# Performance work log

Hardware: AMD Instinct MI355X
Metric: run time of the kernel (lower is better)

The kernel has to match this reference:

```python
import jax, jax.numpy as jnp
import numpy as np

T, B, D, H = 512, 128, 512, 512


def setup_inputs() -> dict:
    key = jax.random.key(0)
    ks = jax.random.split(key, 14)
    s = 0.05
    return {
        "inputs": jax.random.normal(ks[0], (T, B, D), dtype=jnp.float32),
        # gate linears: Linear(D+H, out) -> weight [out, D+H], bias [out]
        "Wf": jax.random.normal(ks[1], (2, D + H), dtype=jnp.float32) * s,
        "bf": jax.random.normal(ks[2], (2,), dtype=jnp.float32) * s,
        "Wi": jax.random.normal(ks[3], (H, D + H), dtype=jnp.float32) * s,
        "bi": jax.random.normal(ks[4], (H,), dtype=jnp.float32) * s,
        "Wu": jax.random.normal(ks[5], (H, D + H), dtype=jnp.float32) * s,
        "bu": jax.random.normal(ks[6], (H,), dtype=jnp.float32) * s,
        "Wo": jax.random.normal(ks[7], (H, D + H), dtype=jnp.float32) * s,
        "bo": jax.random.normal(ks[8], (H,), dtype=jnp.float32) * s,
        # SamplerModule: Linear(2,4) -> Tanh -> Linear(4,2) -> softmax
        "Ws1": jax.random.normal(ks[9], (4, 2), dtype=jnp.float32) * 0.5,
        "bs1": jax.random.normal(ks[10], (4,), dtype=jnp.float32) * 0.5,
        "Ws2": jax.random.normal(ks[11], (2, 4), dtype=jnp.float32) * 0.5,
        "bs2": jax.random.normal(ks[12], (2,), dtype=jnp.float32) * 0.5,
    }


def reference(inputs, Wf, bf, Wi, bi, Wu, bu, Wo, bo, Ws1, bs1, Ws2, bs2):
    Bsz = inputs.shape[1]
    h0 = jnp.zeros((Bsz, H), dtype=inputs.dtype)
    c0 = jnp.zeros((Bsz, H), dtype=inputs.dtype)

    def step(carry, x):
        hx, cx = carry
        combined = jnp.concatenate([x, hx], axis=1)  # [B, D+H]
        f_logits = combined @ Wf.T + bf              # [B, 2]
        hdn = jnp.tanh(f_logits @ Ws1.T + bs1)       # [B, 4]
        f_probs = jax.nn.softmax(hdn @ Ws2.T + bs2, axis=-1)  # [B, 2]
        f = f_probs[:, 0:1]                          # [B, 1] forget gate
        i = jax.nn.sigmoid(combined @ Wi.T + bi)
        g = jnp.tanh(combined @ Wu.T + bu)
        o = jax.nn.sigmoid(combined @ Wo.T + bo)
        cx = f * cx + i * g
        hx = o * jnp.tanh(cx)
        return (hx, cx), hx

    (hx, cx), stacked = jax.lax.scan(step, (h0, c0), inputs)
    return stacked, (hx, cx)
```

## Files before the change

### kernel.cpp

```cpp
#include <hip/hip_runtime.h>
#include <cstdint>

#define TT 512
#define BB 128
#define DD 512
#define HH 512
#define KTOT 1024
#define LDK 1032

typedef short bf16x8 __attribute__((ext_vector_type(8)));
typedef float f32x4 __attribute__((ext_vector_type(4)));

__device__ inline unsigned short f2bfs(float f) {
    unsigned int u = __builtin_bit_cast(unsigned int, f);
    u = (u + 0x7FFFu + ((u >> 16) & 1u)) >> 16;
    return (unsigned short)u;
}

__device__ inline float sigf(float x) { return 1.f / (1.f + __expf(-x)); }
__device__ inline float tanhfast(float x) { return 2.f * sigf(2.f * x) - 1.f; }

__device__ inline bf16x8 load8w(const float* p) {
    const float4* p4 = (const float4*)p;
    float4 a = p4[0], b = p4[1];
    bf16x8 r;
    r[0] = (short)f2bfs(a.x); r[1] = (short)f2bfs(a.y);
    r[2] = (short)f2bfs(a.z); r[3] = (short)f2bfs(a.w);
    r[4] = (short)f2bfs(b.x); r[5] = (short)f2bfs(b.y);
    r[6] = (short)f2bfs(b.z); r[7] = (short)f2bfs(b.w);
    return r;
}

__global__ __launch_bounds__(256, 1) void qlstm_kernel(
    const float* __restrict__ X,
    const float* __restrict__ Wf, const float* __restrict__ bfb,
    const float* __restrict__ Wi, const float* __restrict__ bi,
    const float* __restrict__ Wu, const float* __restrict__ bu,
    const float* __restrict__ Wo, const float* __restrict__ bo,
    const float* __restrict__ Ws1, const float* __restrict__ bs1,
    const float* __restrict__ Ws2, const float* __restrict__ bs2,
    float* __restrict__ out,
    unsigned int* __restrict__ flags,
    unsigned short* __restrict__ hbuf)
{
    const int tid  = threadIdx.x;
    const int bid  = blockIdx.x;
    const int rg   = bid & 7;
    const int cg   = bid >> 3;
    const int b0   = rg * 16;
    const int lane = tid & 63;
    const int wv   = tid >> 6;
    const int qd   = lane >> 4;
    const int nn   = lane & 15;

    __shared__ unsigned short comb[16][LDK];
    __shared__ float pc[4][16][17];

    bf16x8 wfr[32];
    {
        bf16x8 z8;
        #pragma unroll
        for (int j = 0; j < 8; ++j) z8[j] = 0;
        const float* Wg = (wv == 0) ? Wi : (wv == 1) ? Wu : (wv == 2) ? Wo : Wf;
        const size_t row = (wv == 3) ? (size_t)nn : (size_t)(cg * 16 + nn);
        const bool valid = (wv < 3) || (nn < 2);
        #pragma unroll
        for (int kk = 0; kk < 32; ++kk)
            wfr[kk] = valid ? load8w(Wg + row * KTOT + kk * 32 + qd * 8) : z8;
    }

    const int fm = tid >> 4, fn = tid & 15;
    const int gcol = cg * 16 + fn;
    const float bir = bi[gcol], bur = bu[gcol], bor = bo[gcol];
    const float bfr0 = bfb[0], bfr1 = bfb[1];
    float ws1r[8], bs1r[4], ws2r[8];
    #pragma unroll
    for (int j = 0; j < 8; ++j) ws1r[j] = Ws1[j];
    #pragma unroll
    for (int j = 0; j < 4; ++j) bs1r[j] = bs1[j];
    #pragma unroll
    for (int j = 0; j < 8; ++j) ws2r[j] = Ws2[j];
    const float bs2r0 = bs2[0], bs2r1 = bs2[1];

    {
        const float4* xs = (const float4*)(X + (size_t)b0 * DD);
        #pragma unroll
        for (int i = 0; i < 8; ++i) {
            const int v = tid + i * 256;
            float4 f4 = xs[v];
            const int row = v >> 7, col = (v & 127) << 2;
            unsigned short* d = &comb[row][col];
            d[0] = f2bfs(f4.x); d[1] = f2bfs(f4.y);
            d[2] = f2bfs(f4.z); d[3] = f2bfs(f4.w);
        }
        #pragma unroll
        for (int i = 0; i < 16; ++i) {
            const int v = tid + i * 256;
            const int row = v >> 8, c2 = (v & 255) << 1;
            *(unsigned int*)&comb[row][DD + c2] = 0u;
        }
    }

    float cval = 0.f;

    for (int t = 0; t < TT; ++t) {
        __syncthreads();

        const unsigned long long* fl = nullptr;
        unsigned long long fv = ~0ull;
        if (t > 0) {
            fl = (const unsigned long long*)&flags[((t - 1) * 8 + rg) * 128];
            fv = __hip_atomic_load(&fl[lane],
                   __ATOMIC_RELAXED, __HIP_MEMORY_SCOPE_AGENT);
        }

        f32x4 ac0 = {0.f, 0.f, 0.f, 0.f}, ac1 = ac0;
        #pragma unroll
        for (int kk = 0; kk < 16; kk += 2) {
            bf16x8 av0 = *(const bf16x8*)&comb[nn][kk * 32 + qd * 8];
            bf16x8 av1 = *(const bf16x8*)&comb[nn][(kk + 1) * 32 + qd * 8];
            ac0 = __builtin_amdgcn_mfma_f32_16x16x32_bf16(av0, wfr[kk], ac0, 0, 0, 0);
            ac1 = __builtin_amdgcn_mfma_f32_16x16x32_bf16(av1, wfr[kk + 1], ac1, 0, 0, 0);
        }

        if (t > 0) {
            while (__ballot(((unsigned int)fv == 0u) |
                            ((unsigned int)(fv >> 32) == 0u)) != 0ull) {
                __builtin_amdgcn_s_sleep(1);
                fv = __hip_atomic_load(&fl[lane],
                       __ATOMIC_RELAXED, __HIP_MEMORY_SCOPE_AGENT);
            }
            asm volatile("" ::: "memory");
            const unsigned long long* hs = (const unsigned long long*)(hbuf
                + (size_t)((t + 1) & 1) * BB * HH + (size_t)b0 * HH);
            #pragma unroll
            for (int i = 0; i < 8; ++i) {
                unsigned long long u = __hip_atomic_load(&hs[tid + i * 256],
                    __ATOMIC_RELAXED, __HIP_MEMORY_SCOPE_AGENT);
                const int v = tid + i * 256;
                *(unsigned long long*)&comb[v >> 7][DD + ((v & 127) << 2)] = u;
            }
        }
        __syncthreads();

        #pragma unroll
        for (int kk = 16; kk < 32; kk += 2) {
            bf16x8 av0 = *(const bf16x8*)&comb[nn][kk * 32 + qd * 8];
            bf16x8 av1 = *(const bf16x8*)&comb[nn][(kk + 1) * 32 + qd * 8];
            ac0 = __builtin_amdgcn_mfma_f32_16x16x32_bf16(av0, wfr[kk], ac0, 0, 0, 0);
            ac1 = __builtin_amdgcn_mfma_f32_16x16x32_bf16(av1, wfr[kk + 1], ac1, 0, 0, 0);
        }
        #pragma unroll
        for (int r = 0; r < 4; ++r)
            pc[wv][qd * 4 + r][nn] = ac0[r] + ac1[r];
        __syncthreads();

        const float l0 = bfr0 + pc[3][fm][0];
        const float l1 = bfr1 + pc[3][fm][1];
        const float hd0 = tanhfast(ws1r[0] * l0 + ws1r[1] * l1 + bs1r[0]);
        const float hd1 = tanhfast(ws1r[2] * l0 + ws1r[3] * l1 + bs1r[1]);
        const float hd2 = tanhfast(ws1r[4] * l0 + ws1r[5] * l1 + bs1r[2]);
        const float hd3 = tanhfast(ws1r[6] * l0 + ws1r[7] * l1 + bs1r[3]);
        const float s0 = bs2r0 + ws2r[0]*hd0 + ws2r[1]*hd1 + ws2r[2]*hd2 + ws2r[3]*hd3;
        const float s1 = bs2r1 + ws2r[4]*hd0 + ws2r[5]*hd1 + ws2r[6]*hd2 + ws2r[7]*hd3;
        const float fval = sigf(s0 - s1);

        const float iv = sigf(bir + pc[0][fm][fn]);
        const float gv = tanhfast(bur + pc[1][fm][fn]);
        const float ov = sigf(bor + pc[2][fm][fn]);
        cval = fval * cval + iv * gv;
        const float hv = ov * tanhfast(cval);
        const int b = b0 + fm;

        {
            unsigned int ub = (unsigned int)f2bfs(hv);
            unsigned int ob = __shfl_xor(ub, 1);
            if ((fn & 1) == 0) {
                unsigned int* hp = (unsigned int*)(hbuf
                    + (size_t)(t & 1) * BB * HH + (size_t)b * HH + gcol);
                __hip_atomic_store(hp, ub | (ob << 16),
                                   __ATOMIC_RELAXED, __HIP_MEMORY_SCOPE_AGENT);
            }
        }
        asm volatile("s_waitcnt vmcnt(0)" ::: "memory");
        if (lane == 0)
            __hip_atomic_store(&flags[(t * 8 + rg) * 128 + cg * 4 + wv], 1u,
                               __ATOMIC_RELAXED, __HIP_MEMORY_SCOPE_AGENT);

        out[((size_t)t * BB + b) * HH + gcol] = hv;
        if (t == TT - 1) {
            out[(size_t)TT * BB * HH + (size_t)b * HH + gcol] = hv;
            out[(size_t)TT * BB * HH + (size_t)BB * HH + (size_t)b * HH + gcol] = cval;
        }
        {
            const int tn = (t + 1 < TT) ? t + 1 : t;
            const float4* xs = (const float4*)(X + ((size_t)tn * BB + b0) * DD);
            float4 xp[8];
            #pragma unroll
            for (int i = 0; i < 8; ++i) xp[i] = xs[tid + i * 256];
            #pragma unroll
            for (int i = 0; i < 8; ++i) {
                const int v = tid + i * 256;
                const int row = v >> 7, col = (v & 127) << 2;
                unsigned short* d = &comb[row][col];
                d[0] = f2bfs(xp[i].x); d[1] = f2bfs(xp[i].y);
                d[2] = f2bfs(xp[i].z); d[3] = f2bfs(xp[i].w);
            }
        }
    }
}

extern "C" void kernel_launch(void* const* d_in, const int* in_sizes, int n_in,
                              void* d_out, int out_size, void* d_ws, size_t ws_size,
                              hipStream_t stream) {
    const float* X   = (const float*)d_in[0];
    const float* Wf  = (const float*)d_in[1];
    const float* bfb = (const float*)d_in[2];
    const float* Wi  = (const float*)d_in[3];
    const float* bi  = (const float*)d_in[4];
    const float* Wu  = (const float*)d_in[5];
    const float* bu  = (const float*)d_in[6];
    const float* Wo  = (const float*)d_in[7];
    const float* bo  = (const float*)d_in[8];
    const float* Ws1 = (const float*)d_in[9];
    const float* bs1 = (const float*)d_in[10];
    const float* Ws2 = (const float*)d_in[11];
    const float* bs2 = (const float*)d_in[12];
    float* out = (float*)d_out;

    unsigned int*   flags = (unsigned int*)d_ws;
    unsigned short* hbuf  = (unsigned short*)((char*)d_ws + (size_t)TT * 8 * 128 * 4);

    hipMemsetAsync(d_ws, 0, (size_t)TT * 8 * 128 * 4, stream);
    qlstm_kernel<<<dim3(256), dim3(256), 0, stream>>>(
        X, Wf, bfb, Wi, bi, Wu, bu, Wo, bo, Ws1, bs1, Ws2, bs2, out, flags, hbuf);
}
```

Baseline: 2.439 ms.

## Split K across waves, feed MFMA operands from registers instead of LDS

Each wave now computes all four gates over a quarter of the K dimension instead of one gate over full K. The A operands (x and h) are loaded straight from global memory into registers, which removes the comb LDS staging buffer and one __syncthreads per step. The x-part MFMAs for step t+1, plus the flag prefetch, are issued at the end of step t so they overlap the wait on the other blocks. The cost is a cross-wave reduction of partial sums through LDS, and many small scattered global loads of h after each flag wait.

```diff
diff --git a/kernel.cpp b/kernel.cpp
--- a/kernel.cpp
+++ b/kernel.cpp
@@ -6,10 +6,10 @@
 #define DD 512
 #define HH 512
 #define KTOT 1024
-#define LDK 1032
 
 typedef short bf16x8 __attribute__((ext_vector_type(8)));
 typedef float f32x4 __attribute__((ext_vector_type(4)));
+typedef unsigned long long u64t;
 
 __device__ inline unsigned short f2bfs(float f) {
     unsigned int u = __builtin_bit_cast(unsigned int, f);
@@ -53,20 +53,24 @@
     const int qd   = lane >> 4;
     const int nn   = lane & 15;
 
-    __shared__ unsigned short comb[16][LDK];
-    __shared__ float pc[4][16][17];
-
-    bf16x8 wfr[32];
+    __shared__ float pcp[4][4][16][17];
+
+    bf16x8 wfr[4][8];
     {
         bf16x8 z8;
         #pragma unroll
         for (int j = 0; j < 8; ++j) z8[j] = 0;
-        const float* Wg = (wv == 0) ? Wi : (wv == 1) ? Wu : (wv == 2) ? Wo : Wf;
-        const size_t row = (wv == 3) ? (size_t)nn : (size_t)(cg * 16 + nn);
-        const bool valid = (wv < 3) || (nn < 2);
-        #pragma unroll
-        for (int kk = 0; kk < 32; ++kk)
-            wfr[kk] = valid ? load8w(Wg + row * KTOT + kk * 32 + qd * 8) : z8;
+        #pragma unroll
+        for (int g = 0; g < 4; ++g) {
+            const float* Wg = (g == 0) ? Wi : (g == 1) ? Wu : (g == 2) ? Wo : Wf;
+            const size_t row = (g == 3) ? (size_t)nn : (size_t)(cg * 16 + nn);
+            const bool valid = (g < 3) || (nn < 2);
+            #pragma unroll
+            for (int j = 0; j < 8; ++j) {
+                const int kk = (j < 4) ? (wv * 4 + j) : (16 + wv * 4 + (j - 4));
+                wfr[g][j] = valid ? load8w(Wg + row * KTOT + kk * 32 + qd * 8) : z8;
+            }
+        }
     }
 
     const int fm = tid >> 4, fn = tid & 15;
@@ -82,48 +86,27 @@
     for (int j = 0; j < 8; ++j) ws2r[j] = Ws2[j];
     const float bs2r0 = bs2[0], bs2r1 = bs2[1];
 
+    f32x4 ac[4];
+    #pragma unroll
+    for (int g = 0; g < 4; ++g) ac[g] = f32x4{0.f, 0.f, 0.f, 0.f};
     {
-        const float4* xs = (const float4*)(X + (size_t)b0 * DD);
-        #pragma unroll
-        for (int i = 0; i < 8; ++i) {
-            const int v = tid + i * 256;
-            float4 f4 = xs[v];
-            const int row = v >> 7, col = (v & 127) << 2;
-            unsigned short* d = &comb[row][col];
-            d[0] = f2bfs(f4.x); d[1] = f2bfs(f4.y);
-            d[2] = f2bfs(f4.z); d[3] = f2bfs(f4.w);
-        }
-        #pragma unroll
-        for (int i = 0; i < 16; ++i) {
-            const int v = tid + i * 256;
-            const int row = v >> 8, c2 = (v & 255) << 1;
-            *(unsigned int*)&comb[row][DD + c2] = 0u;
-        }
+        bf16x8 xa[4];
+        #pragma unroll
+        for (int j = 0; j < 4; ++j)
+            xa[j] = load8w(X + (size_t)(b0 + nn) * DD + (wv * 4 + j) * 32 + qd * 8);
+        #pragma unroll
+        for (int j = 0; j < 4; ++j)
+            #pragma unroll
+            for (int g = 0; g < 4; ++g)
+                ac[g] = __builtin_amdgcn_mfma_f32_16x16x32_bf16(xa[j], wfr[g][j], ac[g], 0, 0, 0);
     }
 
     float cval = 0.f;
+    u64t  fv   = 0;
 
     for (int t = 0; t < TT; ++t) {
-        __syncthreads();
-
-        const unsigned long long* fl = nullptr;
-        unsigned long long fv = ~0ull;
         if (t > 0) {
-            fl = (const unsigned long long*)&flags[((t - 1) * 8 + rg) * 128];
-            fv = __hip_atomic_load(&fl[lane],
-                   __ATOMIC_RELAXED, __HIP_MEMORY_SCOPE_AGENT);
-        }
-
-        f32x4 ac0 = {0.f, 0.f, 0.f, 0.f}, ac1 = ac0;
-        #pragma unroll
-        for (int kk = 0; kk < 16; kk += 2) {
-            bf16x8 av0 = *(const bf16x8*)&comb[nn][kk * 32 + qd * 8];
-            bf16x8 av1 = *(const bf16x8*)&comb[nn][(kk + 1) * 32 + qd * 8];
-            ac0 = __builtin_amdgcn_mfma_f32_16x16x32_bf16(av0, wfr[kk], ac0, 0, 0, 0);
-            ac1 = __builtin_amdgcn_mfma_f32_16x16x32_bf16(av1, wfr[kk + 1], ac1, 0, 0, 0);
-        }
-
-        if (t > 0) {
+            const u64t* fl = (const u64t*)&flags[((t - 1) * 8 + rg) * 128];
             while (__ballot(((unsigned int)fv == 0u) |
                             ((unsigned int)(fv >> 32) == 0u)) != 0ull) {
                 __builtin_amdgcn_s_sleep(1);
@@ -131,32 +114,45 @@
                        __ATOMIC_RELAXED, __HIP_MEMORY_SCOPE_AGENT);
             }
             asm volatile("" ::: "memory");
-            const unsigned long long* hs = (const unsigned long long*)(hbuf
-                + (size_t)((t + 1) & 1) * BB * HH + (size_t)b0 * HH);
-            #pragma unroll
-            for (int i = 0; i < 8; ++i) {
-                unsigned long long u = __hip_atomic_load(&hs[tid + i * 256],
-                    __ATOMIC_RELAXED, __HIP_MEMORY_SCOPE_AGENT);
-                const int v = tid + i * 256;
-                *(unsigned long long*)&comb[v >> 7][DD + ((v & 127) << 2)] = u;
-            }
-        }
+            const u64t* hb = (const u64t*)(hbuf + (size_t)((t + 1) & 1) * BB * HH);
+            u64t hwv[8];
+            #pragma unroll
+            for (int j = 0; j < 4; ++j) {
+                const u64t* hp = hb + (((b0 + nn) * HH + (wv * 4 + j) * 32 + qd * 8) >> 2);
+                hwv[2 * j]     = __hip_atomic_load(hp,
+                                   __ATOMIC_RELAXED, __HIP_MEMORY_SCOPE_AGENT);
+                hwv[2 * j + 1] = __hip_atomic_load(hp + 1,
+                                   __ATOMIC_RELAXED, __HIP_MEMORY_SCOPE_AGENT);
+            }
+            #pragma unroll
+            for (int j = 0; j < 4; ++j) {
+                bf16x8 ha;
+                ((u64t*)&ha)[0] = hwv[2 * j];
+                ((u64t*)&ha)[1] = hwv[2 * j + 1];
+                #pragma unroll
+                for (int g = 0; g < 4; ++g)
+                    ac[g] = __builtin_amdgcn_mfma_f32_16x16x32_bf16(ha, wfr[g][4 + j], ac[g], 0, 0, 0);
+            }
+        }
+
+        #pragma unroll
+        for (int g = 0; g < 4; ++g)
+            #pragma unroll
+            for (int r = 0; r < 4; ++r)
+                pcp[wv][g][qd * 4 + r][nn] = ac[g][r];
         __syncthreads();
 
-        #pragma unroll
-        for (int kk = 16; kk < 32; kk += 2) {
-            bf16x8 av0 = *(const bf16x8*)&comb[nn][kk * 32 + qd * 8];
-            bf16x8 av1 = *(const bf16x8*)&comb[nn][(kk + 1) * 32 + qd * 8];
-            ac0 = __builtin_amdgcn_mfma_f32_16x16x32_bf16(av0, wfr[kk], ac0, 0, 0, 0);
-            ac1 = __builtin_amdgcn_mfma_f32_16x16x32_bf16(av1, wfr[kk + 1], ac1, 0, 0, 0);
-        }
-        #pragma unroll
-        for (int r = 0; r < 4; ++r)
-            pc[wv][qd * 4 + r][nn] = ac0[r] + ac1[r];
-        __syncthreads();
-
-        const float l0 = bfr0 + pc[3][fm][0];
-        const float l1 = bfr1 + pc[3][fm][1];
+        float s0g = 0.f, s1g = 0.f, s2g = 0.f, sl0 = 0.f, sl1 = 0.f;
+        #pragma unroll
+        for (int w = 0; w < 4; ++w) {
+            s0g += pcp[w][0][fm][fn];
+            s1g += pcp[w][1][fm][fn];
+            s2g += pcp[w][2][fm][fn];
+            sl0 += pcp[w][3][fm][0];
+            sl1 += pcp[w][3][fm][1];
+        }
+        const float l0 = bfr0 + sl0;
+        const float l1 = bfr1 + sl1;
         const float hd0 = tanhfast(ws1r[0] * l0 + ws1r[1] * l1 + bs1r[0]);
         const float hd1 = tanhfast(ws1r[2] * l0 + ws1r[3] * l1 + bs1r[1]);
         const float hd2 = tanhfast(ws1r[4] * l0 + ws1r[5] * l1 + bs1r[2]);
@@ -165,9 +161,9 @@
         const float s1 = bs2r1 + ws2r[4]*hd0 + ws2r[5]*hd1 + ws2r[6]*hd2 + ws2r[7]*hd3;
         const float fval = sigf(s0 - s1);
 
-        const float iv = sigf(bir + pc[0][fm][fn]);
-        const float gv = tanhfast(bur + pc[1][fm][fn]);
-        const float ov = sigf(bor + pc[2][fm][fn]);
+        const float iv = sigf(bir + s0g);
+        const float gv = tanhfast(bur + s1g);
+        const float ov = sigf(bor + s2g);
         cval = fval * cval + iv * gv;
         const float hv = ov * tanhfast(cval);
         const int b = b0 + fm;
@@ -192,20 +188,22 @@
             out[(size_t)TT * BB * HH + (size_t)b * HH + gcol] = hv;
             out[(size_t)TT * BB * HH + (size_t)BB * HH + (size_t)b * HH + gcol] = cval;
         }
-        {
-            const int tn = (t + 1 < TT) ? t + 1 : t;
-            const float4* xs = (const float4*)(X + ((size_t)tn * BB + b0) * DD);
-            float4 xp[8];
-            #pragma unroll
-            for (int i = 0; i < 8; ++i) xp[i] = xs[tid + i * 256];
-            #pragma unroll
-            for (int i = 0; i < 8; ++i) {
-                const int v = tid + i * 256;
-                const int row = v >> 7, col = (v & 127) << 2;
-                unsigned short* d = &comb[row][col];
-                d[0] = f2bfs(xp[i].x); d[1] = f2bfs(xp[i].y);
-                d[2] = f2bfs(xp[i].z); d[3] = f2bfs(xp[i].w);
-            }
+        if (t + 1 < TT) {
+            #pragma unroll
+            for (int g = 0; g < 4; ++g) ac[g] = f32x4{0.f, 0.f, 0.f, 0.f};
+            bf16x8 xa[4];
+            #pragma unroll
+            for (int j = 0; j < 4; ++j)
+                xa[j] = load8w(X + ((size_t)(t + 1) * BB + b0 + nn) * DD
+                               + (wv * 4 + j) * 32 + qd * 8);
+            #pragma unroll
+            for (int j = 0; j < 4; ++j)
+                #pragma unroll
+                for (int g = 0; g < 4; ++g)
+                    ac[g] = __builtin_amdgcn_mfma_f32_16x16x32_bf16(xa[j], wfr[g][j], ac[g], 0, 0, 0);
+            fv = __hip_atomic_load(
+                   &((const u64t*)&flags[(t * 8 + rg) * 128])[lane],
+                   __ATOMIC_RELAXED, __HIP_MEMORY_SCOPE_AGENT);
         }
     }
 }
```

New measurement: 1.980 ms. 18.8% less time.
